# Optimization experiments

Hardware: AMD Instinct MI355X
Metric: run time of the kernel (lower is better)

## Reference

```python
import jax, jax.numpy as jnp
import numpy as np
import math

B, N, D, H = 4, 1024, 256, 8  # batch, points, dim_V, heads
DH = D // H                   # per-head dim = 32
INF = jnp.float32(1e38)


def setup_inputs() -> dict:
    key = jax.random.key(0)
    ks = jax.random.split(key, 16)
    s = 0.02
    inp = {
        "X_lift": jax.random.normal(ks[0], (B, N, 3), jnp.float32),
        "Y_lift": jax.random.normal(ks[1], (B, N, D), jnp.float32),
        "X_pairs": jax.random.normal(ks[2], (B, N, N, 3), jnp.float32),
        "presence_q": (jax.random.uniform(ks[3], (B, N)) < 0.9).astype(jnp.float32),
        "presence_k": (jax.random.uniform(ks[4], (B, N)) < 0.9).astype(jnp.float32),
        # projection weights, stored [in, out]
        "Wq": jax.random.normal(ks[5], (D, D), jnp.float32) * s,
        "bq": jnp.zeros((D,), jnp.float32),
        "Wk": jax.random.normal(ks[6], (D, D), jnp.float32) * s,
        "bk": jnp.zeros((D,), jnp.float32),
        "Wv": jax.random.normal(ks[7], (D, D), jnp.float32) * s,
        "bv": jnp.zeros((D,), jnp.float32),
        "Wo": jax.random.normal(ks[8], (D, D), jnp.float32) * s,
        "bo": jnp.zeros((D,), jnp.float32),
        # per-head location-bias MLPs: Linear(3,3) -> ReLU -> Linear(3,1)
        "Wg1": jax.random.normal(ks[9], (H, 3, 3), jnp.float32) * 0.5,
        "bg1": jnp.zeros((H, 3), jnp.float32),
        "wg2": jax.random.normal(ks[10], (H, 3), jnp.float32) * 0.5,
        "bg2": jnp.zeros((H,), jnp.float32),
    }
    return inp


def reference(X_lift, Y_lift, X_pairs, presence_q, presence_k,
              Wq, bq, Wk, bk, Wv, bv, Wo, bo, Wg1, bg1, wg2, bg2):
    # X_lift is unused by the original forward (keys=queries=values=Y_lift)
    Q = Y_lift @ Wq + bq          # [B,N,D]
    K = Y_lift @ Wk + bk
    V = Y_lift @ Wv + bv

    # split into heads, head-major layout [H,B,N,DH]
    Qh = Q.reshape(B, N, H, DH).transpose(2, 0, 1, 3)
    Kh = K.reshape(B, N, H, DH).transpose(2, 0, 1, 3)
    Vh = V.reshape(B, N, H, DH).transpose(2, 0, 1, 3)

    content = jnp.einsum('hbnd,hbmd->hbnm', Qh, Kh) / math.sqrt(D)

    # per-head pairwise location bias MLP on X_pairs [B,N,N,3]
    hid = jax.nn.relu(jnp.einsum('bnmc,hcd->hbnmd', X_pairs, Wg1)
                      + bg1[:, None, None, None, :])       # [H,B,N,N,3]
    loc = jnp.einsum('hbnmd,hd->hbnm', hid, wg2) + bg2[:, None, None, None]

    logits = content + loc                                  # [H,B,N,N]

    pq = presence_q[None, :, :, None]                       # [1,B,N,1]
    logits = pq * logits - (1.0 - pq) * INF
    pk = presence_k[None, :, None, :]                       # [1,B,1,N]
    logits = pk * logits - (1.0 - pk) * INF

    A = jax.nn.softmax(logits, axis=-1)                     # [H,B,N,N]
    Oh = jnp.einsum('hbnm,hbmd->hbnd', A, Vh)               # [H,B,N,DH]
    O = V + Oh.transpose(1, 2, 0, 3).reshape(B, N, D)       # residual on values
    O = O + jax.nn.relu(O @ Wo + bo)
    return O
```

## Files before the change

kernel.cpp:

```cpp
#include <hip/hip_runtime.h>
#include <hip/hip_bf16.h>
#include <math.h>

typedef __bf16 bf16;
typedef __bf16 bf16x4 __attribute__((ext_vector_type(4)));
typedef __bf16 bf16x8 __attribute__((ext_vector_type(8)));
typedef float f32x2 __attribute__((ext_vector_type(2)));
typedef float f32x4 __attribute__((ext_vector_type(4)));

#define NB 4
#define NN 1024
#define ND 256
#define NH 8
#define INFV 1e38f
#define RTHR2 11.5f
#define LOG2E 1.44269504f
#define ZSPLIT 4

__device__ __forceinline__ f32x4 mfma16(bf16x8 a, bf16x8 b, f32x4 c) {
    return __builtin_amdgcn_mfma_f32_16x16x32_bf16(a, b, c, 0, 0, 0);
}
__device__ __forceinline__ f32x2 sp2(float v) { return f32x2{v, v}; }
__device__ __forceinline__ f32x2 fma2(f32x2 a, float b, f32x2 c) {
    return __builtin_elementwise_fma(a, sp2(b), c);
}
__device__ __forceinline__ float rfl(float x) {
    return __int_as_float(__builtin_amdgcn_readfirstlane(__float_as_int(x)));
}

template<int MODE>
__global__ __launch_bounds__(256)
void gemm_k(const float* __restrict__ A,
            const float* __restrict__ W0, const float* __restrict__ b0,
            const float* __restrict__ W1, const float* __restrict__ b1,
            const float* __restrict__ W2, const float* __restrict__ b2,
            float* __restrict__ Fo2, bf16* __restrict__ G0,
            bf16* __restrict__ G1, bf16* __restrict__ Gt,
            float* __restrict__ Fo1, const bf16* __restrict__ Ab)
{
    const int z = blockIdx.z;
    const float* W    = (z == 0) ? W0 : (z == 1) ? W1 : W2;
    const float* bias = (z == 0) ? b0 : (z == 1) ? b1 : b2;

    const int brow = blockIdx.x * 64;
    const int bcol = blockIdx.y * 64;
    const int t    = threadIdx.x;
    const int lane = t & 63;
    const int w    = t >> 6;
    const int wr   = w >> 1, wc = w & 1;
    const int g    = lane >> 4;
    const int l16  = lane & 15;

    __shared__ bf16 As[64][40];
    __shared__ bf16 Wt[64][40];

    f32x4 acc[2][2];
    #pragma unroll
    for (int i = 0; i < 2; ++i)
        #pragma unroll
        for (int j = 0; j < 2; ++j) acc[i][j] = f32x4{0.f, 0.f, 0.f, 0.f};

    const int ar = t >> 2, aj = (t & 3) * 8;
    const int wcid = t & 63, wk = (t >> 6) * 8;

    for (int k0 = 0; k0 < 256; k0 += 32) {
        if (MODE == 1) {
            *(bf16x8*)&As[ar][aj] =
                *(const bf16x8*)&Ab[(size_t)(brow + ar)*ND + k0 + aj];
        } else {
            const float4 v0 = *(const float4*)&A[(size_t)(brow + ar)*ND + k0 + aj];
            const float4 v1 = *(const float4*)&A[(size_t)(brow + ar)*ND + k0 + aj + 4];
            bf16x8 w8 = { (bf16)v0.x, (bf16)v0.y, (bf16)v0.z, (bf16)v0.w,
                          (bf16)v1.x, (bf16)v1.y, (bf16)v1.z, (bf16)v1.w };
            *(bf16x8*)&As[ar][aj] = w8;
        }
        {
            bf16x8 w8;
            #pragma unroll
            for (int p = 0; p < 8; ++p)
                w8[p] = (bf16)W[(size_t)(k0 + wk + p)*ND + bcol + wcid];
            *(bf16x8*)&Wt[wcid][wk] = w8;
        }
        __syncthreads();

        bf16x8 af[2], bfj[2];
        #pragma unroll
        for (int i = 0; i < 2; ++i) af[i]  = *(const bf16x8*)&As[wr*32 + i*16 + l16][8*g];
        #pragma unroll
        for (int j = 0; j < 2; ++j) bfj[j] = *(const bf16x8*)&Wt[wc*32 + j*16 + l16][8*g];
        #pragma unroll
        for (int j = 0; j < 2; ++j)
            #pragma unroll
            for (int i = 0; i < 2; ++i) acc[i][j] = mfma16(af[i], bfj[j], acc[i][j]);
        __syncthreads();
    }

    #pragma unroll
    for (int j = 0; j < 2; ++j) {
        const int col = bcol + wc*32 + j*16 + l16;
        const float bj = bias[col];
        #pragma unroll
        for (int i = 0; i < 2; ++i) {
            const int row0 = brow + wr*32 + i*16 + 4*g;
            if (MODE == 1) {
                #pragma unroll
                for (int r = 0; r < 4; ++r) {
                    const size_t idx = (size_t)(row0 + r)*ND + col;
                    Fo1[idx] = (float)Ab[idx] + fmaxf(acc[i][j][r] + bj, 0.f);
                }
            } else if (z < 2) {
                bf16* Go = (z == 0) ? G0 : G1;
                #pragma unroll
                for (int r = 0; r < 4; ++r)
                    Go[(size_t)(row0 + r)*ND + col] = (bf16)(acc[i][j][r] + bj);
            } else {
                float vv[4];
                #pragma unroll
                for (int r = 0; r < 4; ++r) {
                    vv[r] = acc[i][j][r] + bj;
                    Fo2[(size_t)(row0 + r)*ND + col] = vv[r];
                }
                const int b2 = row0 >> 10;
                const int n0 = row0 & 1023;
                bf16x4 tv = { (bf16)vv[0], (bf16)vv[1], (bf16)vv[2], (bf16)vv[3] };
                *(bf16x4*)&Gt[((size_t)b2*ND + col)*NN + n0] = tv;
            }
        }
    }
}

__global__ __launch_bounds__(256, 4)
void attn_k(const bf16* __restrict__ Qb, const bf16* __restrict__ Kb,
            const bf16* __restrict__ Vt, const float* __restrict__ Xpg,
            const float* __restrict__ prq, const float* __restrict__ prk,
            const float* __restrict__ Wg1, const float* __restrict__ bg1,
            const float* __restrict__ wg2, const float* __restrict__ bg2,
            float* __restrict__ Ohp, float* __restrict__ ml)
{
    const int yb   = blockIdx.y;
    const int b    = yb >> 1;
    const int hg   = yb & 1;
    const int q0   = blockIdx.x * 16;
    const int z    = blockIdx.z;
    const int mb0  = z * (NN/ZSPLIT);
    const int t    = threadIdx.x;
    const int w    = t >> 6;
    const int h    = hg*4 + w;
    const int lane = t & 63;
    const int g    = lane >> 4;
    const int l16  = lane & 15;
    const int NT   = NN/ZSPLIT/32;

    __shared__ float Xps[2][16*132];
    __shared__ bf16  Ps[4][16][40];

    float g1[3][3], gb1[3], g2v[3], gb2v;
    #pragma unroll
    for (int c = 0; c < 3; ++c)
        #pragma unroll
        for (int d = 0; d < 3; ++d) g1[c][d] = rfl(Wg1[(h*3 + c)*3 + d]);
    #pragma unroll
    for (int d = 0; d < 3; ++d) {
        gb1[d] = rfl(bg1[h*3 + d]);
        g2v[d] = rfl(wg2[h*3 + d]*LOG2E);
    }
    gb2v = rfl(bg2[h]*LOG2E);
    const float sscale = 0.0625f * LOG2E;

    const bf16x8 qf = *(const bf16x8*)&Qb[((size_t)b*NN + q0 + l16)*ND + h*32 + 8*g];

    bool okq[4];
    #pragma unroll
    for (int r = 0; r < 4; ++r)
        okq[r] = prq[b*NN + q0 + 4*g + r] > 0.5f;

    float m_run[4], l_run[4];
    f32x4 oh[2];
    #pragma unroll
    for (int r = 0; r < 4; ++r) { m_run[r] = -INFINITY; l_run[r] = 0.f; }
    oh[0] = f32x4{0.f,0.f,0.f,0.f};
    oh[1] = f32x4{0.f,0.f,0.f,0.f};

    const bf16*  kp0 = &Kb[((size_t)b*NN + mb0 + l16)*ND + h*32 + 8*g];
    const bf16*  kp1 = kp0 + (size_t)16*ND;
    const bf16*  vp0 = &Vt[((size_t)b*ND + h*32 + l16)*NN + mb0 + 8*g];
    const bf16*  vp1 = vp0 + (size_t)16*NN;
    const int    xq  = t >> 5, xm = t & 31;
    const float* xppA = &Xpg[(((size_t)b*NN + q0 + xq)*NN + mb0 + xm)*3];
    const float* xppB = &Xpg[(((size_t)b*NN + q0 + xq + 8)*NN + mb0 + xm)*3];
    const float* pkp  = &prk[(size_t)b*NN + mb0 + l16];

    bf16x8 kf0 = *(const bf16x8*)kp0;
    bf16x8 kf1 = *(const bf16x8*)kp1;
    bf16x8 vf0 = *(const bf16x8*)vp0;
    bf16x8 vf1 = *(const bf16x8*)vp1;
    float xxA = xppA[0], xyA = xppA[1], xzA = xppA[2];
    float xxB = xppB[0], xyB = xppB[1], xzB = xppB[2];
    float pk0 = pkp[0], pk1 = pkp[16];
    {
        *(float4*)&Xps[0][xq*132 + xm*4]       = float4{xxA, xyA, xzA, 0.f};
        *(float4*)&Xps[0][(xq + 8)*132 + xm*4] = float4{xxB, xyB, xzB, 0.f};
    }
    __syncthreads();

    for (int it = 0; it < NT; ++it) {
        const int cur = it & 1;

        bf16x8 kn0, kn1, vn0, vn1;
        float  xnxA, xnyA, xnzA, xnxB, xnyB, xnzB, pn0, pn1;
        if (it + 1 < NT) {
            const int off = (it + 1) * 32;
            kn0 = *(const bf16x8*)(kp0 + (size_t)off*ND);
            kn1 = *(const bf16x8*)(kp1 + (size_t)off*ND);
            vn0 = *(const bf16x8*)(vp0 + off);
            vn1 = *(const bf16x8*)(vp1 + off);
            xnxA = xppA[(size_t)off*3];
            xnyA = xppA[(size_t)off*3 + 1];
            xnzA = xppA[(size_t)off*3 + 2];
            xnxB = xppB[(size_t)off*3];
            xnyB = xppB[(size_t)off*3 + 1];
            xnzB = xppB[(size_t)off*3 + 2];
            pn0 = pkp[off]; pn1 = pkp[off + 16];
        }

        const f32x4 zero = {0.f,0.f,0.f,0.f};
        f32x4 s[2];
        s[0] = mfma16(qf, kf0, zero);
        s[1] = mfma16(qf, kf1, zero);

        const bool okk0 = pk0 > 0.5f;
        const bool okk1 = pk1 > 0.5f;

        float lv[2][4];
        #pragma unroll
        for (int mg = 0; mg < 2; ++mg) {
            const bool okkm = mg ? okk1 : okk0;
            const int m = mg*16 + l16;
            #pragma unroll
            for (int rp = 0; rp < 2; ++rp) {
                const int q = 4*g + 2*rp;
                const float4 xa = *(const float4*)&Xps[cur][q*132 + m*4];
                const float4 xb = *(const float4*)&Xps[cur][(q+1)*132 + m*4];
                const f32x2 vx = {xa.x, xb.x};
                const f32x2 vy = {xa.y, xb.y};
                const f32x2 vz = {xa.z, xb.z};
                f32x2 h0 = fma2(vz, g1[2][0], fma2(vy, g1[1][0], fma2(vx, g1[0][0], sp2(gb1[0]))));
                f32x2 h1 = fma2(vz, g1[2][1], fma2(vy, g1[1][1], fma2(vx, g1[0][1], sp2(gb1[1]))));
                f32x2 h2 = fma2(vz, g1[2][2], fma2(vy, g1[1][2], fma2(vx, g1[0][2], sp2(gb1[2]))));
                const f32x2 zz = {0.f, 0.f};
                h0 = __builtin_elementwise_max(h0, zz);
                h1 = __builtin_elementwise_max(h1, zz);
                h2 = __builtin_elementwise_max(h2, zz);
                f32x2 loc = fma2(h2, g2v[2], fma2(h1, g2v[1], fma2(h0, g2v[0], sp2(gb2v))));
                const f32x2 s2 = { s[mg][2*rp], s[mg][2*rp+1] };
                const f32x2 y = fma2(s2, sscale, loc);
                lv[mg][2*rp]   = (okq[2*rp]   && okkm) ? y.x : -INFV;
                lv[mg][2*rp+1] = (okq[2*rp+1] && okkm) ? y.y : -INFV;
            }
        }

        float pm[4];
        #pragma unroll
        for (int r = 0; r < 4; ++r) pm[r] = fmaxf(lv[0][r], lv[1][r]);
        const bool cond = (pm[0] <= m_run[0] + RTHR2) && (pm[1] <= m_run[1] + RTHR2)
                       && (pm[2] <= m_run[2] + RTHR2) && (pm[3] <= m_run[3] + RTHR2);
        if (!__all((int)cond)) {
            #pragma unroll
            for (int r = 0; r < 4; ++r) {
                float mx = pm[r];
                mx = fmaxf(mx, __shfl_xor(mx, 1));
                mx = fmaxf(mx, __shfl_xor(mx, 2));
                mx = fmaxf(mx, __shfl_xor(mx, 4));
                mx = fmaxf(mx, __shfl_xor(mx, 8));
                const float mnew = fmaxf(m_run[r], mx);
                const float corr = exp2f(m_run[r] - mnew);
                l_run[r] *= corr;
                oh[0][r] *= corr;
                oh[1][r] *= corr;
                m_run[r] = mnew;
            }
        }
        #pragma unroll
        for (int r = 0; r < 4; ++r) {
            const float p0 = exp2f(lv[0][r] - m_run[r]);
            const float p1 = exp2f(lv[1][r] - m_run[r]);
            Ps[w][4*g + r][l16]      = (bf16)p0;
            Ps[w][4*g + r][16 + l16] = (bf16)p1;
            l_run[r] += p0 + p1;
        }

        const bf16x8 pf = *(const bf16x8*)&Ps[w][l16][8*g];
        oh[0] = mfma16(pf, vf0, oh[0]);
        oh[1] = mfma16(pf, vf1, oh[1]);

        if (it + 1 < NT) {
            *(float4*)&Xps[cur ^ 1][xq*132 + xm*4]       = float4{xnxA, xnyA, xnzA, 0.f};
            *(float4*)&Xps[cur ^ 1][(xq + 8)*132 + xm*4] = float4{xnxB, xnyB, xnzB, 0.f};
            kf0 = kn0; kf1 = kn1; vf0 = vn0; vf1 = vn1;
            pk0 = pn0; pk1 = pn1;
        }
        __syncthreads();
    }

    #pragma unroll
    for (int r = 0; r < 4; ++r) {
        float ls = l_run[r];
        ls += __shfl_xor(ls, 1);
        ls += __shfl_xor(ls, 2);
        ls += __shfl_xor(ls, 4);
        ls += __shfl_xor(ls, 8);
        const int n = q0 + 4*g + r;
        #pragma unroll
        for (int dg = 0; dg < 2; ++dg) {
            const int col = h*32 + dg*16 + l16;
            Ohp[(((size_t)z*NB + b)*NN + n)*ND + col] = oh[dg][r];
        }
        if (l16 == 0) {
            const size_t mi = ((((size_t)z*NB + b)*NN + n)*NH + h)*2;
            ml[mi]   = m_run[r];
            ml[mi+1] = ls;
        }
    }
}

__global__ __launch_bounds__(256)
void comb_k(const float* __restrict__ Ohp, const float* __restrict__ ml,
            const float* __restrict__ Vf, bf16* __restrict__ O1b)
{
    const int idx = blockIdx.x * 256 + threadIdx.x;
    const int dq = idx & 63;
    const int bn = idx >> 6;
    const int d0 = dq * 4;
    const int h  = dq >> 3;

    const size_t base = ((size_t)bn*NH + h)*2;
    const size_t zstr = (size_t)NB*NN*NH*2;
    float mz[ZSPLIT], lz[ZSPLIT];
    float M = -INFINITY;
    #pragma unroll
    for (int zi = 0; zi < ZSPLIT; ++zi) {
        mz[zi] = ml[base + zi*zstr];
        lz[zi] = ml[base + zi*zstr + 1];
        M = fmaxf(M, mz[zi]);
    }
    float wz[ZSPLIT], den = 0.f;
    #pragma unroll
    for (int zi = 0; zi < ZSPLIT; ++zi) {
        wz[zi] = exp2f(mz[zi] - M);
        den = fmaf(lz[zi], wz[zi], den);
    }
    const float inv = 1.f / den;

    const size_t e = (size_t)bn*ND + d0;
    f32x4 num = {0.f,0.f,0.f,0.f};
    #pragma unroll
    for (int zi = 0; zi < ZSPLIT; ++zi) {
        const f32x4 o = *(const f32x4*)&Ohp[e + (size_t)zi*NB*NN*ND];
        #pragma unroll
        for (int r = 0; r < 4; ++r) num[r] = fmaf(o[r], wz[zi], num[r]);
    }
    const f32x4 vf = *(const f32x4*)&Vf[e];
    bf16x4 out;
    #pragma unroll
    for (int r = 0; r < 4; ++r) out[r] = (bf16)(vf[r] + num[r]*inv);
    *(bf16x4*)&O1b[e] = out;
}

extern "C" void kernel_launch(void* const* d_in, const int* in_sizes, int n_in,
                              void* d_out, int out_size, void* d_ws, size_t ws_size,
                              hipStream_t stream)
{
    const float* Y   = (const float*)d_in[1];
    const float* Xp  = (const float*)d_in[2];
    const float* prq = (const float*)d_in[3];
    const float* prk = (const float*)d_in[4];
    const float* Wq  = (const float*)d_in[5];
    const float* bq  = (const float*)d_in[6];
    const float* Wk  = (const float*)d_in[7];
    const float* bk  = (const float*)d_in[8];
    const float* Wv  = (const float*)d_in[9];
    const float* bv  = (const float*)d_in[10];
    const float* Wo  = (const float*)d_in[11];
    const float* bo  = (const float*)d_in[12];
    const float* Wg1 = (const float*)d_in[13];
    const float* bg1 = (const float*)d_in[14];
    const float* wg2 = (const float*)d_in[15];
    const float* bg2 = (const float*)d_in[16];
    float* out = (float*)d_out;

    const size_t BND = (size_t)NB * NN * ND;
    float* Vf  = (float*)d_ws;
    float* Ohp = Vf + BND;
    float* ml  = Ohp + (size_t)ZSPLIT*BND;
    bf16*  Qb  = (bf16*)(ml + (size_t)ZSPLIT*NB*NN*NH*2);
    bf16*  Kb  = Qb + BND;
    bf16*  Vt  = Kb + BND;
    bf16*  O1b = Qb;

    gemm_k<0><<<dim3(64, 4, 3), 256, 0, stream>>>(
        Y, Wq, bq, Wk, bk, Wv, bv,
        Vf, Qb, Kb, Vt, nullptr, nullptr);

    attn_k<<<dim3(NN/16, NB*2, ZSPLIT), 256, 0, stream>>>(
        Qb, Kb, Vt, Xp, prq, prk, Wg1, bg1, wg2, bg2, Ohp, ml);

    comb_k<<<dim3(1024), 256, 0, stream>>>(Ohp, ml, Vf, O1b);

    gemm_k<1><<<dim3(64, 4, 1), 256, 0, stream>>>(
        nullptr, Wo, bo, Wo, bo, Wo, bo,
        nullptr, nullptr, nullptr, nullptr, out, O1b);
}
```

Measured before the change: 70.56 us.

## Process 64-key tiles per barrier and halve the key-dimension split

After: 76.91 us. 9.0% more time.

```diff
diff --git a/kernel.cpp b/kernel.cpp
--- a/kernel.cpp
+++ b/kernel.cpp
@@ -15,7 +15,7 @@
 #define INFV 1e38f
 #define RTHR2 11.5f
 #define LOG2E 1.44269504f
-#define ZSPLIT 4
+#define ZSPLIT 2
 
 __device__ __forceinline__ f32x4 mfma16(bf16x8 a, bf16x8 b, f32x4 c) {
     return __builtin_amdgcn_mfma_f32_16x16x32_bf16(a, b, c, 0, 0, 0);
@@ -129,7 +129,7 @@
     }
 }
 
-__global__ __launch_bounds__(256, 4)
+__global__ __launch_bounds__(256, 2)
 void attn_k(const bf16* __restrict__ Qb, const bf16* __restrict__ Kb,
             const bf16* __restrict__ Vt, const float* __restrict__ Xpg,
             const float* __restrict__ prq, const float* __restrict__ prk,
@@ -149,9 +149,9 @@
     const int lane = t & 63;
     const int g    = lane >> 4;
     const int l16  = lane & 15;
-    const int NT   = NN/ZSPLIT/32;
-
-    __shared__ float Xps[2][16*132];
+    const int NT   = NN/ZSPLIT/64;
+
+    __shared__ float Xps[2][16*260];
     __shared__ bf16  Ps[4][16][40];
 
     float g1[3][3], gb1[3], g2v[3], gb2v;
@@ -181,123 +181,210 @@
     oh[0] = f32x4{0.f,0.f,0.f,0.f};
     oh[1] = f32x4{0.f,0.f,0.f,0.f};
 
-    const bf16*  kp0 = &Kb[((size_t)b*NN + mb0 + l16)*ND + h*32 + 8*g];
-    const bf16*  kp1 = kp0 + (size_t)16*ND;
+    const bf16*  kpb = &Kb[((size_t)b*NN + mb0 + l16)*ND + h*32 + 8*g];
     const bf16*  vp0 = &Vt[((size_t)b*ND + h*32 + l16)*NN + mb0 + 8*g];
     const bf16*  vp1 = vp0 + (size_t)16*NN;
     const int    xq  = t >> 5, xm = t & 31;
-    const float* xppA = &Xpg[(((size_t)b*NN + q0 + xq)*NN + mb0 + xm)*3];
-    const float* xppB = &Xpg[(((size_t)b*NN + q0 + xq + 8)*NN + mb0 + xm)*3];
-    const float* pkp  = &prk[(size_t)b*NN + mb0 + l16];
-
-    bf16x8 kf0 = *(const bf16x8*)kp0;
-    bf16x8 kf1 = *(const bf16x8*)kp1;
-    bf16x8 vf0 = *(const bf16x8*)vp0;
-    bf16x8 vf1 = *(const bf16x8*)vp1;
-    float xxA = xppA[0], xyA = xppA[1], xzA = xppA[2];
-    float xxB = xppB[0], xyB = xppB[1], xzB = xppB[2];
-    float pk0 = pkp[0], pk1 = pkp[16];
+    const float* xpA = &Xpg[(((size_t)b*NN + q0 + xq)*NN + mb0 + xm)*3];
+    const float* xpB = xpA + (size_t)8*NN*3;
+    const float* pkp = &prk[(size_t)b*NN + mb0 + l16];
+
+    bf16x8 kf0 = *(const bf16x8*)(kpb);
+    bf16x8 kf1 = *(const bf16x8*)(kpb + (size_t)16*ND);
+    bf16x8 kf2 = *(const bf16x8*)(kpb + (size_t)32*ND);
+    bf16x8 kf3 = *(const bf16x8*)(kpb + (size_t)48*ND);
     {
-        *(float4*)&Xps[0][xq*132 + xm*4]       = float4{xxA, xyA, xzA, 0.f};
-        *(float4*)&Xps[0][(xq + 8)*132 + xm*4] = float4{xxB, xyB, xzB, 0.f};
+        float a0 = xpA[0],    a1 = xpA[1],    a2 = xpA[2];
+        float b0 = xpA[96],   b1 = xpA[97],   b2 = xpA[98];
+        float c0 = xpB[0],    c1 = xpB[1],    c2 = xpB[2];
+        float d0 = xpB[96],   d1 = xpB[97],   d2 = xpB[98];
+        *(float4*)&Xps[0][xq*260 + xm*4]            = float4{a0, a1, a2, 0.f};
+        *(float4*)&Xps[0][xq*260 + (xm + 32)*4]     = float4{b0, b1, b2, 0.f};
+        *(float4*)&Xps[0][(xq + 8)*260 + xm*4]        = float4{c0, c1, c2, 0.f};
+        *(float4*)&Xps[0][(xq + 8)*260 + (xm + 32)*4] = float4{d0, d1, d2, 0.f};
     }
     __syncthreads();
 
+    #pragma unroll 1
     for (int it = 0; it < NT; ++it) {
         const int cur = it & 1;
-
-        bf16x8 kn0, kn1, vn0, vn1;
-        float  xnxA, xnyA, xnzA, xnxB, xnyB, xnzB, pn0, pn1;
+        const int m0  = it * 64;
+
+        bf16x8 kn0, kn1, kn2, kn3;
+        float na0, na1, na2, nb0, nb1, nb2, nc0, nc1, nc2, nd0, nd1, nd2;
         if (it + 1 < NT) {
-            const int off = (it + 1) * 32;
-            kn0 = *(const bf16x8*)(kp0 + (size_t)off*ND);
-            kn1 = *(const bf16x8*)(kp1 + (size_t)off*ND);
-            vn0 = *(const bf16x8*)(vp0 + off);
-            vn1 = *(const bf16x8*)(vp1 + off);
-            xnxA = xppA[(size_t)off*3];
-            xnyA = xppA[(size_t)off*3 + 1];
-            xnzA = xppA[(size_t)off*3 + 2];
-            xnxB = xppB[(size_t)off*3];
-            xnyB = xppB[(size_t)off*3 + 1];
-            xnzB = xppB[(size_t)off*3 + 2];
-            pn0 = pkp[off]; pn1 = pkp[off + 16];
-        }
-
-        const f32x4 zero = {0.f,0.f,0.f,0.f};
-        f32x4 s[2];
-        s[0] = mfma16(qf, kf0, zero);
-        s[1] = mfma16(qf, kf1, zero);
-
-        const bool okk0 = pk0 > 0.5f;
-        const bool okk1 = pk1 > 0.5f;
-
-        float lv[2][4];
-        #pragma unroll
-        for (int mg = 0; mg < 2; ++mg) {
-            const bool okkm = mg ? okk1 : okk0;
-            const int m = mg*16 + l16;
-            #pragma unroll
-            for (int rp = 0; rp < 2; ++rp) {
-                const int q = 4*g + 2*rp;
-                const float4 xa = *(const float4*)&Xps[cur][q*132 + m*4];
-                const float4 xb = *(const float4*)&Xps[cur][(q+1)*132 + m*4];
-                const f32x2 vx = {xa.x, xb.x};
-                const f32x2 vy = {xa.y, xb.y};
-                const f32x2 vz = {xa.z, xb.z};
-                f32x2 h0 = fma2(vz, g1[2][0], fma2(vy, g1[1][0], fma2(vx, g1[0][0], sp2(gb1[0]))));
-                f32x2 h1 = fma2(vz, g1[2][1], fma2(vy, g1[1][1], fma2(vx, g1[0][1], sp2(gb1[1]))));
-                f32x2 h2 = fma2(vz, g1[2][2], fma2(vy, g1[1][2], fma2(vx, g1[0][2], sp2(gb1[2]))));
-                const f32x2 zz = {0.f, 0.f};
-                h0 = __builtin_elementwise_max(h0, zz);
-                h1 = __builtin_elementwise_max(h1, zz);
-                h2 = __builtin_elementwise_max(h2, zz);
-                f32x2 loc = fma2(h2, g2v[2], fma2(h1, g2v[1], fma2(h0, g2v[0], sp2(gb2v))));
-                const f32x2 s2 = { s[mg][2*rp], s[mg][2*rp+1] };
-                const f32x2 y = fma2(s2, sscale, loc);
-                lv[mg][2*rp]   = (okq[2*rp]   && okkm) ? y.x : -INFV;
-                lv[mg][2*rp+1] = (okq[2*rp+1] && okkm) ? y.y : -INFV;
-            }
-        }
-
-        float pm[4];
-        #pragma unroll
-        for (int r = 0; r < 4; ++r) pm[r] = fmaxf(lv[0][r], lv[1][r]);
-        const bool cond = (pm[0] <= m_run[0] + RTHR2) && (pm[1] <= m_run[1] + RTHR2)
-                       && (pm[2] <= m_run[2] + RTHR2) && (pm[3] <= m_run[3] + RTHR2);
-        if (!__all((int)cond)) {
+            const size_t ko = (size_t)(m0 + 64)*ND;
+            kn0 = *(const bf16x8*)(kpb + ko);
+            kn1 = *(const bf16x8*)(kpb + ko + (size_t)16*ND);
+            kn2 = *(const bf16x8*)(kpb + ko + (size_t)32*ND);
+            kn3 = *(const bf16x8*)(kpb + ko + (size_t)48*ND);
+            const size_t xo = (size_t)(m0 + 64)*3;
+            na0 = xpA[xo];      na1 = xpA[xo+1];    na2 = xpA[xo+2];
+            nb0 = xpA[xo+96];   nb1 = xpA[xo+97];   nb2 = xpA[xo+98];
+            nc0 = xpB[xo];      nc1 = xpB[xo+1];    nc2 = xpB[xo+2];
+            nd0 = xpB[xo+96];   nd1 = xpB[xo+97];   nd2 = xpB[xo+98];
+        }
+
+        {
+            const int msub = m0;
+            const bf16x8 vf0 = *(const bf16x8*)(vp0 + msub);
+            const bf16x8 vf1 = *(const bf16x8*)(vp1 + msub);
+            const float pk0 = pkp[msub], pk1 = pkp[msub + 16];
+
+            const f32x4 zero = {0.f,0.f,0.f,0.f};
+            f32x4 s[2];
+            s[0] = mfma16(qf, kf0, zero);
+            s[1] = mfma16(qf, kf1, zero);
+
+            const bool okk0 = pk0 > 0.5f;
+            const bool okk1 = pk1 > 0.5f;
+
+            float lv[2][4];
+            #pragma unroll
+            for (int mg = 0; mg < 2; ++mg) {
+                const bool okkm = mg ? okk1 : okk0;
+                const int m = mg*16 + l16;
+                #pragma unroll
+                for (int rp = 0; rp < 2; ++rp) {
+                    const int q = 4*g + 2*rp;
+                    const float4 xa = *(const float4*)&Xps[cur][q*260 + m*4];
+                    const float4 xb = *(const float4*)&Xps[cur][(q+1)*260 + m*4];
+                    const f32x2 vx = {xa.x, xb.x};
+                    const f32x2 vy = {xa.y, xb.y};
+                    const f32x2 vz = {xa.z, xb.z};
+                    f32x2 h0 = fma2(vz, g1[2][0], fma2(vy, g1[1][0], fma2(vx, g1[0][0], sp2(gb1[0]))));
+                    f32x2 h1 = fma2(vz, g1[2][1], fma2(vy, g1[1][1], fma2(vx, g1[0][1], sp2(gb1[1]))));
+                    f32x2 h2 = fma2(vz, g1[2][2], fma2(vy, g1[1][2], fma2(vx, g1[0][2], sp2(gb1[2]))));
+                    const f32x2 zz = {0.f, 0.f};
+                    h0 = __builtin_elementwise_max(h0, zz);
+                    h1 = __builtin_elementwise_max(h1, zz);
+                    h2 = __builtin_elementwise_max(h2, zz);
+                    f32x2 loc = fma2(h2, g2v[2], fma2(h1, g2v[1], fma2(h0, g2v[0], sp2(gb2v))));
+                    const f32x2 s2 = { s[mg][2*rp], s[mg][2*rp+1] };
+                    const f32x2 y = fma2(s2, sscale, loc);
+                    lv[mg][2*rp]   = (okq[2*rp]   && okkm) ? y.x : -INFV;
+                    lv[mg][2*rp+1] = (okq[2*rp+1] && okkm) ? y.y : -INFV;
+                }
+            }
+
+            float pm[4];
+            #pragma unroll
+            for (int r = 0; r < 4; ++r) pm[r] = fmaxf(lv[0][r], lv[1][r]);
+            const bool cond = (pm[0] <= m_run[0] + RTHR2) && (pm[1] <= m_run[1] + RTHR2)
+                           && (pm[2] <= m_run[2] + RTHR2) && (pm[3] <= m_run[3] + RTHR2);
+            if (!__all((int)cond)) {
+                #pragma unroll
+                for (int r = 0; r < 4; ++r) {
+                    float mx = pm[r];
+                    mx = fmaxf(mx, __shfl_xor(mx, 1));
+                    mx = fmaxf(mx, __shfl_xor(mx, 2));
+                    mx = fmaxf(mx, __shfl_xor(mx, 4));
+                    mx = fmaxf(mx, __shfl_xor(mx, 8));
+                    const float mnew = fmaxf(m_run[r], mx);
+                    const float corr = exp2f(m_run[r] - mnew);
+                    l_run[r] *= corr;
+                    oh[0][r] *= corr;
+                    oh[1][r] *= corr;
+                    m_run[r] = mnew;
+                }
+            }
             #pragma unroll
             for (int r = 0; r < 4; ++r) {
-                float mx = pm[r];
-                mx = fmaxf(mx, __shfl_xor(mx, 1));
-                mx = fmaxf(mx, __shfl_xor(mx, 2));
-                mx = fmaxf(mx, __shfl_xor(mx, 4));
-                mx = fmaxf(mx, __shfl_xor(mx, 8));
-                const float mnew = fmaxf(m_run[r], mx);
-                const float corr = exp2f(m_run[r] - mnew);
-                l_run[r] *= corr;
-                oh[0][r] *= corr;
-                oh[1][r] *= corr;
-                m_run[r] = mnew;
-            }
-        }
-        #pragma unroll
-        for (int r = 0; r < 4; ++r) {
-            const float p0 = exp2f(lv[0][r] - m_run[r]);
-            const float p1 = exp2f(lv[1][r] - m_run[r]);
-            Ps[w][4*g + r][l16]      = (bf16)p0;
-            Ps[w][4*g + r][16 + l16] = (bf16)p1;
-            l_run[r] += p0 + p1;
-        }
-
-        const bf16x8 pf = *(const bf16x8*)&Ps[w][l16][8*g];
-        oh[0] = mfma16(pf, vf0, oh[0]);
-        oh[1] = mfma16(pf, vf1, oh[1]);
+                const float p0 = exp2f(lv[0][r] - m_run[r]);
+                const float p1 = exp2f(lv[1][r] - m_run[r]);
+                Ps[w][4*g + r][l16]      = (bf16)p0;
+                Ps[w][4*g + r][16 + l16] = (bf16)p1;
+                l_run[r] += p0 + p1;
+            }
+
+            const bf16x8 pf = *(const bf16x8*)&Ps[w][l16][8*g];
+            oh[0] = mfma16(pf, vf0, oh[0]);
+            oh[1] = mfma16(pf, vf1, oh[1]);
+        }
+
+        {
+            const int msub = m0 + 32;
+            const bf16x8 vf0 = *(const bf16x8*)(vp0 + msub);
+            const bf16x8 vf1 = *(const bf16x8*)(vp1 + msub);
+            const float pk0 = pkp[msub], pk1 = pkp[msub + 16];
+
+            const f32x4 zero = {0.f,0.f,0.f,0.f};
+            f32x4 s[2];
+            s[0] = mfma16(qf, kf2, zero);
+            s[1] = mfma16(qf, kf3, zero);
+
+            const bool okk0 = pk0 > 0.5f;
+            const bool okk1 = pk1 > 0.5f;
+
+            float lv[2][4];
+            #pragma unroll
+            for (int mg = 0; mg < 2; ++mg) {
+                const bool okkm = mg ? okk1 : okk0;
+                const int m = 32 + mg*16 + l16;
+                #pragma unroll
+                for (int rp = 0; rp < 2; ++rp) {
+                    const int q = 4*g + 2*rp;
+                    const float4 xa = *(const float4*)&Xps[cur][q*260 + m*4];
+                    const float4 xb = *(const float4*)&Xps[cur][(q+1)*260 + m*4];
+                    const f32x2 vx = {xa.x, xb.x};
+                    const f32x2 vy = {xa.y, xb.y};
+                    const f32x2 vz = {xa.z, xb.z};
+                    f32x2 h0 = fma2(vz, g1[2][0], fma2(vy, g1[1][0], fma2(vx, g1[0][0], sp2(gb1[0]))));
+                    f32x2 h1 = fma2(vz, g1[2][1], fma2(vy, g1[1][1], fma2(vx, g1[0][1], sp2(gb1[1]))));
+                    f32x2 h2 = fma2(vz, g1[2][2], fma2(vy, g1[1][2], fma2(vx, g1[0][2], sp2(gb1[2]))));
+                    const f32x2 zz = {0.f, 0.f};
+                    h0 = __builtin_elementwise_max(h0, zz);
+                    h1 = __builtin_elementwise_max(h1, zz);
+                    h2 = __builtin_elementwise_max(h2, zz);
+                    f32x2 loc = fma2(h2, g2v[2], fma2(h1, g2v[1], fma2(h0, g2v[0], sp2(gb2v))));
+                    const f32x2 s2 = { s[mg][2*rp], s[mg][2*rp+1] };
+                    const f32x2 y = fma2(s2, sscale, loc);
+                    lv[mg][2*rp]   = (okq[2*rp]   && okkm) ? y.x : -INFV;
+                    lv[mg][2*rp+1] = (okq[2*rp+1] && okkm) ? y.y : -INFV;
+                }
+            }
+
+            float pm[4];
+            #pragma unroll
+            for (int r = 0; r < 4; ++r) pm[r] = fmaxf(lv[0][r], lv[1][r]);
+            const bool cond = (pm[0] <= m_run[0] + RTHR2) && (pm[1] <= m_run[1] + RTHR2)
+                           && (pm[2] <= m_run[2] + RTHR2) && (pm[3] <= m_run[3] + RTHR2);
+            if (!__all((int)cond)) {
+                #pragma unroll
+                for (int r = 0; r < 4; ++r) {
+                    float mx = pm[r];
+                    mx = fmaxf(mx, __shfl_xor(mx, 1));
+                    mx = fmaxf(mx, __shfl_xor(mx, 2));
+                    mx = fmaxf(mx, __shfl_xor(mx, 4));
+                    mx = fmaxf(mx, __shfl_xor(mx, 8));
+                    const float mnew = fmaxf(m_run[r], mx);
+                    const float corr = exp2f(m_run[r] - mnew);
+                    l_run[r] *= corr;
+                    oh[0][r] *= corr;
+                    oh[1][r] *= corr;
+                    m_run[r] = mnew;
+                }
+            }
+            #pragma unroll
+            for (int r = 0; r < 4; ++r) {
+                const float p0 = exp2f(lv[0][r] - m_run[r]);
+                const float p1 = exp2f(lv[1][r] - m_run[r]);
+                Ps[w][4*g + r][l16]      = (bf16)p0;
+                Ps[w][4*g + r][16 + l16] = (bf16)p1;
+                l_run[r] += p0 + p1;
+            }
+
+            const bf16x8 pf = *(const bf16x8*)&Ps[w][l16][8*g];
+            oh[0] = mfma16(pf, vf0, oh[0]);
+            oh[1] = mfma16(pf, vf1, oh[1]);
+        }
 
         if (it + 1 < NT) {
-            *(float4*)&Xps[cur ^ 1][xq*132 + xm*4]       = float4{xnxA, xnyA, xnzA, 0.f};
-            *(float4*)&Xps[cur ^ 1][(xq + 8)*132 + xm*4] = float4{xnxB, xnyB, xnzB, 0.f};
-            kf0 = kn0; kf1 = kn1; vf0 = vn0; vf1 = vn1;
-            pk0 = pn0; pk1 = pn1;
+            *(float4*)&Xps[cur ^ 1][xq*260 + xm*4]            = float4{na0, na1, na2, 0.f};
+            *(float4*)&Xps[cur ^ 1][xq*260 + (xm + 32)*4]     = float4{nb0, nb1, nb2, 0.f};
+            *(float4*)&Xps[cur ^ 1][(xq + 8)*260 + xm*4]        = float4{nc0, nc1, nc2, 0.f};
+            *(float4*)&Xps[cur ^ 1][(xq + 8)*260 + (xm + 32)*4] = float4{nd0, nd1, nd2, 0.f};
+            kf0 = kn0; kf1 = kn1; kf2 = kn2; kf3 = kn3;
         }
         __syncthreads();
     }
```
